# Optimization experiments

Hardware: AMD Instinct MI355X
Metric: run time of the kernel (lower is better)

Reference implementation:

```python
import jax, jax.numpy as jnp
import numpy as np

N_QUBITS = 14
N_LAYERS = 4
N_CLASSES = 10
BATCH = 1024


def apply_1q(state, gate, wire):
    """Apply a 2x2 gate ([2,2] shared or [B,2,2] batched) to `wire` of state [B,2,...,2]."""
    s = jnp.moveaxis(state, wire + 1, -1)
    shp = s.shape
    s = s.reshape(shp[0], -1, 2)
    if gate.ndim == 3:
        s = jnp.einsum('bij,bkj->bki', gate, s)
    else:
        s = jnp.einsum('ij,bkj->bki', gate, s)
    return jnp.moveaxis(s.reshape(shp), -1, wire + 1)


def apply_cnot(state, c, t):
    s = jnp.moveaxis(state, (c + 1, t + 1), (-2, -1))
    s = jnp.stack([s[..., 0, :], s[..., 1, ::-1]], axis=-2)
    return jnp.moveaxis(s, (-2, -1), (c + 1, t + 1))


def simulate(x, q_params):
    """Batched statevector sim of: RY(x_i) embed -> BasicEntanglerLayers(RX + CNOT ring) -> <Z_i>."""
    B, n = x.shape
    state = jnp.zeros((B,) + (2,) * n, jnp.complex64)
    state = state.at[(slice(None),) + (0,) * n].set(1.0)

    # RY(x_i) on each wire (angles batched per sample)
    c, s = jnp.cos(0.5 * x), jnp.sin(0.5 * x)
    for w in range(n):
        g = jnp.stack([jnp.stack([c[:, w], -s[:, w]], -1),
                       jnp.stack([s[:, w], c[:, w]], -1)], -2).astype(jnp.complex64)  # [B,2,2]
        state = apply_1q(state, g, w)

    # BasicEntanglerLayers: per layer RX(weights[l,i]) on every wire, then CNOT ring
    cw, sw = jnp.cos(0.5 * q_params), jnp.sin(0.5 * q_params)
    n_layers = q_params.shape[0]
    for l in range(n_layers):
        for w in range(n):
            cc = cw[l, w].astype(jnp.complex64)
            isw = (-1j) * sw[l, w].astype(jnp.complex64)
            g = jnp.stack([jnp.stack([cc, isw]), jnp.stack([isw, cc])])  # [2,2] RX
            state = apply_1q(state, g, w)
        if n == 2:
            state = apply_cnot(state, 0, 1)
        else:
            for w in range(n):
                state = apply_cnot(state, w, (w + 1) % n)

    # <Z_i> = P(bit_i=0) - P(bit_i=1)
    p = jnp.abs(state) ** 2  # [B,2,...,2] real
    axes_all = tuple(range(1, n + 1))
    z = []
    for w in range(n):
        pw = jnp.sum(p, axis=tuple(a for a in axes_all if a != w + 1))  # [B,2]
        z.append(pw[:, 0] - pw[:, 1])
    return jnp.stack(z, -1).astype(jnp.float32)  # [B, n]


def setup_inputs() -> dict:
    key = jax.random.key(0)
    k1, k2, k3, k4 = jax.random.split(key, 4)
    x = jax.random.normal(k1, (BATCH, N_QUBITS), dtype=jnp.float32)
    q_params = 0.01 * jax.random.normal(k2, (N_LAYERS, N_QUBITS), dtype=jnp.float32)
    fc_w = jax.random.normal(k3, (N_CLASSES, N_QUBITS), dtype=jnp.float32) / np.sqrt(N_QUBITS)
    fc_b = jax.random.normal(k4, (N_CLASSES,), dtype=jnp.float32) * 0.01
    return {"x": x, "q_params": q_params, "fc_w": fc_w, "fc_b": fc_b}


def reference(x, q_params, fc_w, fc_b):
    q_out = simulate(x, q_params)            # [B, n_qubits]
    logits = q_out @ fc_w.T + fc_b           # [B, n_classes]
    return logits
```

## Files before the change

### kernel.cpp

```cpp
#include <hip/hip_runtime.h>
#include <hip/hip_fp16.h>
#include <math.h>


#define NQ 14
#define NLAYERS 4
#define NCLASSES 10
#define BLOCK 512

typedef _Float16 f16;
typedef _Float16 f16x8 __attribute__((ext_vector_type(8)));
typedef _Float16 f16x4 __attribute__((ext_vector_type(4)));
typedef float f32x4 __attribute__((ext_vector_type(4)));
typedef unsigned int u32;
typedef u32 u32x4 __attribute__((ext_vector_type(4)));

__device__ __forceinline__ f32x4 mf(f16x8 a, f16x8 b, f32x4 c) {
  return __builtin_amdgcn_mfma_f32_16x16x32_f16(a, b, c, 0, 0, 0);
}

__device__ __forceinline__ int finv5(int n) {
  n ^= ((n >> 3) & 1) << 4;
  n ^= ((n >> 2) & 1) << 3;
  n ^= ((n >> 1) & 1) << 2;
  n ^= (n & 1) << 1;
  return n;
}
__device__ __forceinline__ int finv3(int n) {
  n ^= ((n >> 2) & 1) << 3;
  n ^= ((n >> 1) & 1) << 2;
  n ^= (n & 1) << 1;
  return n;
}

__device__ __forceinline__ void splitB(f16x8 b, int s, f16x8& br, f16x8& bi) {
  u32x4 u = __builtin_bit_cast(u32x4, b);
  const u32 m0 = s ? 0xFFFF0000u : 0x0000FFFFu;
  const u32 m1 = s ? 0x0000FFFFu : 0xFFFF0000u;
  u32x4 r;
  r[0] = u[0] & m0; r[1] = u[1] & m1; r[2] = u[2] & m1; r[3] = u[3] & m0;
  u32x4 ii;
  ii[0] = u[0] ^ r[0]; ii[1] = u[1] ^ r[1]; ii[2] = u[2] ^ r[2]; ii[3] = u[3] ^ r[3];
  br = __builtin_bit_cast(f16x8, r);
  bi = __builtin_bit_cast(f16x8, ii);
}

__device__ __forceinline__ void build32(f16* Bc, const float* qc, const float* qs,
                                        int base, int tid) {
  const float c0 = qc[base], c1 = qc[base+1], c2 = qc[base+2], c3 = qc[base+3], c4 = qc[base+4];
  const float s0 = qs[base], s1 = qs[base+1], s2 = qs[base+2], s3 = qs[base+3], s4 = qs[base+4];
#pragma unroll
  for (int e = tid; e < 1024; e += BLOCK) {
    const int n = e >> 5, k = e & 31;
    const int d = finv5(n) ^ k;
    float mag = ((d & 1) ? s0 : c0) * ((d & 2) ? s1 : c1);
    mag *= ((d & 4) ? s2 : c2) * ((d & 8) ? s3 : c3);
    mag *= ((d & 16) ? s4 : c4);
    const int t = __popc(d) & 3;
    Bc[n * 32 + k] = (f16)((t == 1 || t == 2) ? -mag : mag);
  }
}

__device__ __forceinline__ void buildC(f16* Bc, const float* qc, const float* qs,
                                       int base, int tid) {
  const float c0 = qc[base], c1 = qc[base+1], c2 = qc[base+2], c3 = qc[base+3];
  const float s0 = qs[base], s1 = qs[base+1], s2 = qs[base+2], s3 = qs[base+3];
  if (tid < 512) {
    const int n = tid >> 5, k = tid & 31;
    float v = 0.f;
    if (k < 16) {
      const int d = finv3(n) ^ k;
      float mag = ((d & 1) ? s0 : c0) * ((d & 2) ? s1 : c1);
      mag *= ((d & 4) ? s2 : c2) * ((d & 8) ? s3 : c3);
      const int t = __popc(d) & 3;
      v = (t == 1 || t == 2) ? -mag : mag;
    }
    Bc[n * 32 + k] = (f16)v;
  }
}

template<bool CTRL>
__device__ __forceinline__ void pass32(f16* __restrict__ reP, f16* __restrict__ imP,
                                       const f16* __restrict__ Bc, int tid) {
  const int lane = tid & 63, wave = tid >> 6;
  const int q = lane >> 4, cc = lane & 15;
  int n0 = cc, n1 = cc | 16;
  if (CTRL && wave >= 4) { n0 ^= 31; n1 ^= 31; }
  const int pq = (0x6 >> q) & 1;
  f16x8 br0, bi0, br1, bi1;
  {
    const f16x8 b0 = *(const f16x8*)(Bc + n0 * 32 + 8 * q);
    const f16x8 b1 = *(const f16x8*)(Bc + n1 * 32 + 8 * q);
    splitB(b0, ((n0 >> 4) ^ pq) & 1, br0, bi0);
    splitB(b1, ((n1 >> 4) ^ pq) & 1, br1, bi1);
  }
  f16x4 outR[8], outI[8];
#pragma unroll
  for (int i = 0; i < 4; ++i) {
    const int mt = wave * 4 + i;
    const int pA = ((mt * 16 + cc) * 32 + 8 * q) ^ ((mt & 7) << 3);
    const f16x8 Ar = *(const f16x8*)(reP + pA);
    const f16x8 Ai = *(const f16x8*)(imP + pA);
    const f16x8 nAi = -Ai;
#pragma unroll
    for (int nt = 0; nt < 2; ++nt) {
      const f16x8 br = nt ? br1 : br0;
      const f16x8 bi = nt ? bi1 : bi0;
      f32x4 aR = {0.f, 0.f, 0.f, 0.f}, aI = {0.f, 0.f, 0.f, 0.f};
      aR = mf(Ar, br, aR); aR = mf(nAi, bi, aR);
      aI = mf(Ar, bi, aI); aI = mf(Ai, br, aI);
      outR[i * 2 + nt] = __builtin_convertvector(aR, f16x4);
      outI[i * 2 + nt] = __builtin_convertvector(aI, f16x4);
    }
  }
  __syncthreads();
#pragma unroll
  for (int i = 0; i < 4; ++i) {
#pragma unroll
    for (int nt = 0; nt < 2; ++nt) {
      const int n5 = nt * 16 + cc;
      const int rr = (wave * 4 + i) * 16 + 4 * q;
      const int pS = (rr | (n5 << 9)) ^ ((n5 & 7) << 3);
      *(f16x4*)(reP + pS) = outR[i * 2 + nt];
      *(f16x4*)(imP + pS) = outI[i * 2 + nt];
    }
  }
}

template<bool FINAL>
__device__ __forceinline__ void passC(f16* __restrict__ reP, f16* __restrict__ imP,
                                      const f16* __restrict__ Bc, int tid,
                                      float* __restrict__ zloc) {
  const int lane = tid & 63, wave = tid >> 6;
  const int q = lane >> 4, cc = lane & 15;
  int n0 = cc;
  if (wave >= 4) n0 ^= 15;
  const int pq = (0x6 >> q) & 1;
  f16x8 br, bi;
  {
    const f16x8 b = *(const f16x8*)(Bc + n0 * 32 + 8 * q);
    splitB(b, ((n0 >> 3) ^ pq) & 1, br, bi);
  }
  f16x4 outR[8], outI[8];
#pragma unroll
  for (int i = 0; i < 8; ++i) {
    const int mt = wave * 8 + i;
    const int pA = ((mt * 16 + cc) * 16 + 8 * (q & 1)) ^ (((mt >> 1) & 7) << 3);
    const f16x8 Ar = *(const f16x8*)(reP + pA);
    const f16x8 Ai = *(const f16x8*)(imP + pA);
    const f16x8 nAi = -Ai;
    f32x4 aR = {0.f, 0.f, 0.f, 0.f}, aI = {0.f, 0.f, 0.f, 0.f};
    aR = mf(Ar, br, aR); aR = mf(nAi, bi, aR);
    aI = mf(Ar, bi, aI); aI = mf(Ai, br, aI);
    if constexpr (FINAL) {
      float p0 = aR[0]*aR[0] + aI[0]*aI[0];
      float p1 = aR[1]*aR[1] + aI[1]*aI[1];
      float p2 = aR[2]*aR[2] + aI[2]*aI[2];
      float p3 = aR[3]*aR[3] + aI[3]*aI[3];
      if (cc & 8) { float t = p0; p0 = p1; p1 = t; t = p2; p2 = p3; p3 = t; }
      const float ps = p0 + p1 + p2 + p3;
      zloc[0] += (p0 - p1) + (p2 - p3);
      zloc[1] += (p0 + p1) - (p2 + p3);
      zloc[2] += (q & 1) ? -ps : ps;
      zloc[3] += (q & 2) ? -ps : ps;
#pragma unroll
      for (int w = 0; w < 6; ++w) zloc[4 + w] += ((mt >> w) & 1) ? -ps : ps;
#pragma unroll
      for (int w = 0; w < 4; ++w) zloc[10 + w] += ((cc >> w) & 1) ? -ps : ps;
    } else {
      if (cc & 8) {
        f32x4 tR = aR, tI = aI;
        aR[0] = tR[1]; aR[1] = tR[0]; aR[2] = tR[3]; aR[3] = tR[2];
        aI[0] = tI[1]; aI[1] = tI[0]; aI[2] = tI[3]; aI[3] = tI[2];
      }
      outR[i] = __builtin_convertvector(aR, f16x4);
      outI[i] = __builtin_convertvector(aI, f16x4);
    }
  }
  if constexpr (!FINAL) {
    __syncthreads();
#pragma unroll
    for (int i = 0; i < 8; ++i) {
      const int rr = (wave * 8 + i) * 16 + 4 * q;
      const int nI = rr | (cc << 10);
      const int pS = nI ^ ((((rr >> 9) | ((cc & 3) << 1)) & 7) << 3);
      *(f16x4*)(reP + pS) = outR[i];
      *(f16x4*)(imP + pS) = outI[i];
    }
  }
}

__global__ __launch_bounds__(BLOCK, 4) void qsim_kernel(
    const float* __restrict__ x, const float* __restrict__ qp,
    const float* __restrict__ fcw, const float* __restrict__ fcb,
    float* __restrict__ out) {
  extern __shared__ unsigned char smem[];
  f16* reP = (f16*)smem;
  f16* imP = reP + 16384;
  unsigned char* scr = (unsigned char*)(imP + 16384);
  f16* Bc = (f16*)scr;
  float* qc = (float*)(scr + 2048);
  float* qs = qc + 56;
  float* xc = qs + 56;
  float* xs = xc + 14;

  const int b = blockIdx.x;
  const int tid = threadIdx.x;

  if (tid < NQ) {
    float sv, cv; sincosf(0.5f * x[b * NQ + tid], &sv, &cv);
    xc[tid] = cv; xs[tid] = sv;
  } else if (tid >= 64 && tid < 64 + NLAYERS * NQ) {
    const int k = tid - 64;
    float sv, cv; sincosf(0.5f * qp[k], &sv, &cv);
    qc[k] = cv; qs[k] = sv;
  }
  __syncthreads();

  float* Flo  = (float*)scr;
  float* psi  = Flo + 32;
  float* PsiR = psi + 32;
  float* PsiI = PsiR + 32;
  if (tid < 32) {
    float f = 1.f;
#pragma unroll
    for (int j = 0; j < 5; ++j) f *= ((tid >> j) & 1) ? xs[5 + j] : xc[5 + j];
    Flo[tid] = f;
  } else if (tid < 64) {
    const int k = tid - 32;
    float f = 1.f;
#pragma unroll
    for (int j = 0; j < 5; ++j) f *= ((k >> j) & 1) ? xs[j] : xc[j];
    psi[k] = f;
  }
  __syncthreads();
  if (tid < 32) {
    const float c0 = qc[0], c1 = qc[1], c2 = qc[2], c3 = qc[3], c4 = qc[4];
    const float s0 = qs[0], s1 = qs[1], s2 = qs[2], s3 = qs[3], s4 = qs[4];
    const int a = finv5(tid);
    float ar = 0.f, ai = 0.f;
    for (int k = 0; k < 32; ++k) {
      const int d = a ^ k;
      float mag = ((d & 1) ? s0 : c0) * ((d & 2) ? s1 : c1);
      mag *= ((d & 4) ? s2 : c2) * ((d & 8) ? s3 : c3);
      mag *= ((d & 16) ? s4 : c4);
      mag *= psi[k];
      const int t = __popc(d) & 3;
      if (t == 0) ar += mag; else if (t == 1) ai -= mag;
      else if (t == 2) ar -= mag; else ai += mag;
    }
    PsiR[tid] = ar; PsiI[tid] = ai;
  }
  __syncthreads();
  {
    float fhi = 1.f;
#pragma unroll
    for (int j = 0; j < 4; ++j) fhi *= ((tid >> j) & 1) ? xs[10 + j] : xc[10 + j];
    const float cr = fhi * PsiR[tid >> 4], ci = fhi * PsiI[tid >> 4];
    const int pconst = ((tid >> 4) & 7) << 3;
#pragma unroll
    for (int kb = 0; kb < 4; ++kb) {
      f16x8 hr, hi;
#pragma unroll
      for (int j = 0; j < 8; ++j) {
        const float F = Flo[8 * kb + j];
        hr[j] = (f16)(F * cr);
        hi[j] = (f16)(F * ci);
      }
      const int pb = (tid * 32 + 8 * kb) ^ pconst;
      *(f16x8*)(reP + pb) = hr;
      *(f16x8*)(imP + pb) = hi;
    }
  }
  __syncthreads();

  build32(Bc, qc, qs, 0 * NQ + 5, tid);  __syncthreads();
  pass32<true>(reP, imP, Bc, tid);       __syncthreads();
  buildC(Bc, qc, qs, 0 * NQ + 10, tid);  __syncthreads();
  passC<false>(reP, imP, Bc, tid, nullptr); __syncthreads();
#pragma unroll
  for (int l = 1; l < 3; ++l) {
    build32(Bc, qc, qs, l * NQ + 0, tid);  __syncthreads();
    pass32<false>(reP, imP, Bc, tid);      __syncthreads();
    build32(Bc, qc, qs, l * NQ + 5, tid);  __syncthreads();
    pass32<true>(reP, imP, Bc, tid);       __syncthreads();
    buildC(Bc, qc, qs, l * NQ + 10, tid);  __syncthreads();
    passC<false>(reP, imP, Bc, tid, nullptr); __syncthreads();
  }
  build32(Bc, qc, qs, 3 * NQ + 0, tid);  __syncthreads();
  pass32<false>(reP, imP, Bc, tid);      __syncthreads();
  build32(Bc, qc, qs, 3 * NQ + 5, tid);  __syncthreads();
  pass32<true>(reP, imP, Bc, tid);       __syncthreads();
  buildC(Bc, qc, qs, 3 * NQ + 10, tid);  __syncthreads();

  float zloc[NQ];
#pragma unroll
  for (int w = 0; w < NQ; ++w) zloc[w] = 0.f;
  passC<true>(reP, imP, Bc, tid, zloc);
  __syncthreads();

  float* zpart = (float*)scr;
  float* zbuf  = zpart + 112;
#pragma unroll
  for (int w = 0; w < NQ; ++w) {
#pragma unroll
    for (int off = 32; off > 0; off >>= 1)
      zloc[w] += __shfl_down(zloc[w], off, 64);
  }
  const int wave = tid >> 6, lane = tid & 63;
  if (lane == 0) {
#pragma unroll
    for (int w = 0; w < NQ; ++w) zpart[wave * NQ + w] = zloc[w];
  }
  __syncthreads();
  if (tid < NQ) {
    float a = 0.f;
#pragma unroll
    for (int v = 0; v < 8; ++v) a += zpart[v * NQ + tid];
    zbuf[tid] = a;
  }
  __syncthreads();
  if (tid < NCLASSES) {
    float acc = fcb[tid];
#pragma unroll
    for (int w = 0; w < NQ; ++w) acc = fmaf(zbuf[w], fcw[tid * NQ + w], acc);
    out[b * NCLASSES + tid] = acc;
  }
}

extern "C" void kernel_launch(void* const* d_in, const int* in_sizes, int n_in,
                              void* d_out, int out_size, void* d_ws, size_t ws_size,
                              hipStream_t stream) {
  const float* x   = (const float*)d_in[0];
  const float* qp  = (const float*)d_in[1];
  const float* fcw = (const float*)d_in[2];
  const float* fcb = (const float*)d_in[3];
  float* out = (float*)d_out;
  const int B = in_sizes[0] / NQ;

  const size_t shmem = 65536 + 2048 + 448 + 112;
  (void)hipFuncSetAttribute((const void*)qsim_kernel,
                            hipFuncAttributeMaxDynamicSharedMemorySize, (int)shmem);
  qsim_kernel<<<B, BLOCK, shmem, stream>>>(x, qp, fcw, fcb, out);
}
```

Baseline: 146.1 us.

## Double-buffer gate matrices and overlap gate build with MFMA passes; new LDS swizzle

Gate matrices are now built into a second LDS buffer inside each pass, between the MFMA compute and the barrier, instead of in separate build-then-sync phases. This removes roughly one barrier per pass and hides the build ALU work behind MFMA latency. The state and gate LDS layouts are reorganised with a new XOR swizzle to change bank-conflict behaviour on the A loads and scattered stores. The negation moves from the A operand to the B fragment so it is computed once per pass. The risks are higher register pressure and layout-index bugs.

```diff
diff --git a/kernel.cpp b/kernel.cpp
--- a/kernel.cpp
+++ b/kernel.cpp
@@ -18,6 +18,7 @@
 __device__ __forceinline__ f32x4 mf(f16x8 a, f16x8 b, f32x4 c) {
   return __builtin_amdgcn_mfma_f32_16x16x32_f16(a, b, c, 0, 0, 0);
 }
+__device__ __forceinline__ int swz(int t) { return ((t ^ (t >> 3)) & 7) << 3; }
 
 __device__ __forceinline__ int finv5(int n) {
   n ^= ((n >> 3) & 1) << 4;
@@ -57,10 +58,9 @@
     mag *= ((d & 4) ? s2 : c2) * ((d & 8) ? s3 : c3);
     mag *= ((d & 16) ? s4 : c4);
     const int t = __popc(d) & 3;
-    Bc[n * 32 + k] = (f16)((t == 1 || t == 2) ? -mag : mag);
-  }
-}
-
+    Bc[256 * (k >> 3) + 8 * n + (k & 7)] = (f16)((t == 1 || t == 2) ? -mag : mag);
+  }
+}
 __device__ __forceinline__ void buildC(f16* Bc, const float* qc, const float* qs,
                                        int base, int tid) {
   const float c0 = qc[base], c1 = qc[base+1], c2 = qc[base+2], c3 = qc[base+3];
@@ -75,13 +75,15 @@
       const int t = __popc(d) & 3;
       v = (t == 1 || t == 2) ? -mag : mag;
     }
-    Bc[n * 32 + k] = (f16)v;
-  }
-}
-
-template<bool CTRL>
+    Bc[256 * (k >> 3) + 8 * n + (k & 7)] = (f16)v;
+  }
+}
+
+template<bool CTRL, bool STORE_C, int BUILD>
 __device__ __forceinline__ void pass32(f16* __restrict__ reP, f16* __restrict__ imP,
-                                       const f16* __restrict__ Bc, int tid) {
+                                       const f16* __restrict__ BcR, f16* __restrict__ BcW,
+                                       const float* __restrict__ qc,
+                                       const float* __restrict__ qs, int bbase, int tid) {
   const int lane = tid & 63, wave = tid >> 6;
   const int q = lane >> 4, cc = lane & 15;
   int n0 = cc, n1 = cc | 16;
@@ -89,47 +91,61 @@
   const int pq = (0x6 >> q) & 1;
   f16x8 br0, bi0, br1, bi1;
   {
-    const f16x8 b0 = *(const f16x8*)(Bc + n0 * 32 + 8 * q);
-    const f16x8 b1 = *(const f16x8*)(Bc + n1 * 32 + 8 * q);
+    const f16x8 b0 = *(const f16x8*)(BcR + 256 * q + 8 * n0);
+    const f16x8 b1 = *(const f16x8*)(BcR + 256 * q + 8 * n1);
     splitB(b0, ((n0 >> 4) ^ pq) & 1, br0, bi0);
     splitB(b1, ((n1 >> 4) ^ pq) & 1, br1, bi1);
   }
+  const f16x8 nbi0 = -bi0, nbi1 = -bi1;
   f16x4 outR[8], outI[8];
 #pragma unroll
   for (int i = 0; i < 4; ++i) {
     const int mt = wave * 4 + i;
-    const int pA = ((mt * 16 + cc) * 32 + 8 * q) ^ ((mt & 7) << 3);
+    const int pA = mt * 512 + ((128 * q + 8 * cc) ^ swz(mt));
     const f16x8 Ar = *(const f16x8*)(reP + pA);
     const f16x8 Ai = *(const f16x8*)(imP + pA);
-    const f16x8 nAi = -Ai;
-#pragma unroll
-    for (int nt = 0; nt < 2; ++nt) {
-      const f16x8 br = nt ? br1 : br0;
-      const f16x8 bi = nt ? bi1 : bi0;
-      f32x4 aR = {0.f, 0.f, 0.f, 0.f}, aI = {0.f, 0.f, 0.f, 0.f};
-      aR = mf(Ar, br, aR); aR = mf(nAi, bi, aR);
-      aI = mf(Ar, bi, aI); aI = mf(Ai, br, aI);
-      outR[i * 2 + nt] = __builtin_convertvector(aR, f16x4);
-      outI[i * 2 + nt] = __builtin_convertvector(aI, f16x4);
-    }
-  }
+    {
+      f32x4 aR = {0.f,0.f,0.f,0.f}, aI = {0.f,0.f,0.f,0.f};
+      aR = mf(Ar, br0, aR); aR = mf(Ai, nbi0, aR);
+      aI = mf(Ar, bi0, aI); aI = mf(Ai, br0, aI);
+      outR[i * 2 + 0] = __builtin_convertvector(aR, f16x4);
+      outI[i * 2 + 0] = __builtin_convertvector(aI, f16x4);
+    }
+    {
+      f32x4 aR = {0.f,0.f,0.f,0.f}, aI = {0.f,0.f,0.f,0.f};
+      aR = mf(Ar, br1, aR); aR = mf(Ai, nbi1, aR);
+      aI = mf(Ar, bi1, aI); aI = mf(Ai, br1, aI);
+      outR[i * 2 + 1] = __builtin_convertvector(aR, f16x4);
+      outI[i * 2 + 1] = __builtin_convertvector(aI, f16x4);
+    }
+  }
+  if constexpr (BUILD == 1) build32(BcW, qc, qs, bbase, tid);
+  else if constexpr (BUILD == 2) buildC(BcW, qc, qs, bbase, tid);
   __syncthreads();
 #pragma unroll
   for (int i = 0; i < 4; ++i) {
+    const int mt = wave * 4 + i;
 #pragma unroll
     for (int nt = 0; nt < 2; ++nt) {
       const int n5 = nt * 16 + cc;
-      const int rr = (wave * 4 + i) * 16 + 4 * q;
-      const int pS = (rr | (n5 << 9)) ^ ((n5 & 7) << 3);
+      int pS;
+      if constexpr (STORE_C) {
+        const int tC = (mt >> 4) + 2 * n5;
+        pS = tC * 256 + ((128 * (q >> 1) + 8 * (mt & 15) + 4 * (q & 1)) ^ swz(tC));
+      } else {
+        pS = n5 * 512 + ((128 * (2 * (mt & 1) + (q >> 1)) + 8 * (mt >> 1) + 4 * (q & 1)) ^ swz(n5));
+      }
       *(f16x4*)(reP + pS) = outR[i * 2 + nt];
       *(f16x4*)(imP + pS) = outI[i * 2 + nt];
     }
   }
 }
 
-template<bool FINAL>
+template<bool FINAL, int BUILD>
 __device__ __forceinline__ void passC(f16* __restrict__ reP, f16* __restrict__ imP,
-                                      const f16* __restrict__ Bc, int tid,
+                                      const f16* __restrict__ BcR, f16* __restrict__ BcW,
+                                      const float* __restrict__ qc,
+                                      const float* __restrict__ qs, int bbase, int tid,
                                       float* __restrict__ zloc) {
   const int lane = tid & 63, wave = tid >> 6;
   const int q = lane >> 4, cc = lane & 15;
@@ -138,19 +154,19 @@
   const int pq = (0x6 >> q) & 1;
   f16x8 br, bi;
   {
-    const f16x8 b = *(const f16x8*)(Bc + n0 * 32 + 8 * q);
+    const f16x8 b = *(const f16x8*)(BcR + 256 * q + 8 * n0);
     splitB(b, ((n0 >> 3) ^ pq) & 1, br, bi);
   }
+  const f16x8 nbi = -bi;
   f16x4 outR[8], outI[8];
 #pragma unroll
   for (int i = 0; i < 8; ++i) {
-    const int mt = wave * 8 + i;
-    const int pA = ((mt * 16 + cc) * 16 + 8 * (q & 1)) ^ (((mt >> 1) & 7) << 3);
+    const int mtC = wave * 8 + i;
+    const int pA = mtC * 256 + ((128 * (q & 1) + 8 * cc) ^ swz(mtC));
     const f16x8 Ar = *(const f16x8*)(reP + pA);
     const f16x8 Ai = *(const f16x8*)(imP + pA);
-    const f16x8 nAi = -Ai;
-    f32x4 aR = {0.f, 0.f, 0.f, 0.f}, aI = {0.f, 0.f, 0.f, 0.f};
-    aR = mf(Ar, br, aR); aR = mf(nAi, bi, aR);
+    f32x4 aR = {0.f,0.f,0.f,0.f}, aI = {0.f,0.f,0.f,0.f};
+    aR = mf(Ar, br, aR); aR = mf(Ai, nbi, aR);
     aI = mf(Ar, bi, aI); aI = mf(Ai, br, aI);
     if constexpr (FINAL) {
       float p0 = aR[0]*aR[0] + aI[0]*aI[0];
@@ -164,7 +180,7 @@
       zloc[2] += (q & 1) ? -ps : ps;
       zloc[3] += (q & 2) ? -ps : ps;
 #pragma unroll
-      for (int w = 0; w < 6; ++w) zloc[4 + w] += ((mt >> w) & 1) ? -ps : ps;
+      for (int w = 0; w < 6; ++w) zloc[4 + w] += ((mtC >> w) & 1) ? -ps : ps;
 #pragma unroll
       for (int w = 0; w < 4; ++w) zloc[10 + w] += ((cc >> w) & 1) ? -ps : ps;
     } else {
@@ -177,13 +193,15 @@
       outI[i] = __builtin_convertvector(aI, f16x4);
     }
   }
+  if constexpr (BUILD == 1) build32(BcW, qc, qs, bbase, tid);
   if constexpr (!FINAL) {
     __syncthreads();
 #pragma unroll
     for (int i = 0; i < 8; ++i) {
-      const int rr = (wave * 8 + i) * 16 + 4 * q;
-      const int nI = rr | (cc << 10);
-      const int pS = nI ^ ((((rr >> 9) | ((cc & 3) << 1)) & 7) << 3);
+      const int mtC = wave * 8 + i;
+      const int tP = 2 * cc + (mtC >> 5);
+      const int pS = tP * 512 +
+          ((128 * (2 * (mtC & 1) + (q >> 1)) + 8 * ((mtC >> 1) & 15) + 4 * (q & 1)) ^ swz(tP));
       *(f16x4*)(reP + pS) = outR[i];
       *(f16x4*)(imP + pS) = outI[i];
     }
@@ -197,9 +215,9 @@
   extern __shared__ unsigned char smem[];
   f16* reP = (f16*)smem;
   f16* imP = reP + 16384;
-  unsigned char* scr = (unsigned char*)(imP + 16384);
-  f16* Bc = (f16*)scr;
-  float* qc = (float*)(scr + 2048);
+  f16* Bc0 = imP + 16384;
+  f16* Bc1 = Bc0 + 1024;
+  float* qc = (float*)(Bc1 + 1024);
   float* qs = qc + 56;
   float* xc = qs + 56;
   float* xs = xc + 14;
@@ -217,10 +235,11 @@
   }
   __syncthreads();
 
-  float* Flo  = (float*)scr;
+  float* Flo  = (float*)Bc1;
   float* psi  = Flo + 32;
   float* PsiR = psi + 32;
   float* PsiI = PsiR + 32;
+  build32(Bc0, qc, qs, 0 * NQ + 5, tid);
   if (tid < 32) {
     float f = 1.f;
 #pragma unroll
@@ -257,7 +276,8 @@
 #pragma unroll
     for (int j = 0; j < 4; ++j) fhi *= ((tid >> j) & 1) ? xs[10 + j] : xc[10 + j];
     const float cr = fhi * PsiR[tid >> 4], ci = fhi * PsiI[tid >> 4];
-    const int pconst = ((tid >> 4) & 7) << 3;
+    const int t = tid >> 4;
+    const int sz = swz(t);
 #pragma unroll
     for (int kb = 0; kb < 4; ++kb) {
       f16x8 hr, hi;
@@ -267,39 +287,31 @@
         hr[j] = (f16)(F * cr);
         hi[j] = (f16)(F * ci);
       }
-      const int pb = (tid * 32 + 8 * kb) ^ pconst;
+      const int pb = t * 512 + ((128 * kb + 8 * (tid & 15)) ^ sz);
       *(f16x8*)(reP + pb) = hr;
       *(f16x8*)(imP + pb) = hi;
     }
   }
   __syncthreads();
 
-  build32(Bc, qc, qs, 0 * NQ + 5, tid);  __syncthreads();
-  pass32<true>(reP, imP, Bc, tid);       __syncthreads();
-  buildC(Bc, qc, qs, 0 * NQ + 10, tid);  __syncthreads();
-  passC<false>(reP, imP, Bc, tid, nullptr); __syncthreads();
-#pragma unroll
-  for (int l = 1; l < 3; ++l) {
-    build32(Bc, qc, qs, l * NQ + 0, tid);  __syncthreads();
-    pass32<false>(reP, imP, Bc, tid);      __syncthreads();
-    build32(Bc, qc, qs, l * NQ + 5, tid);  __syncthreads();
-    pass32<true>(reP, imP, Bc, tid);       __syncthreads();
-    buildC(Bc, qc, qs, l * NQ + 10, tid);  __syncthreads();
-    passC<false>(reP, imP, Bc, tid, nullptr); __syncthreads();
-  }
-  build32(Bc, qc, qs, 3 * NQ + 0, tid);  __syncthreads();
-  pass32<false>(reP, imP, Bc, tid);      __syncthreads();
-  build32(Bc, qc, qs, 3 * NQ + 5, tid);  __syncthreads();
-  pass32<true>(reP, imP, Bc, tid);       __syncthreads();
-  buildC(Bc, qc, qs, 3 * NQ + 10, tid);  __syncthreads();
+  pass32<true,  true,  2>(reP, imP, Bc0, Bc1, qc, qs, 0*NQ+10, tid); __syncthreads();
+  passC <false, 1>(reP, imP, Bc1, Bc0, qc, qs, 1*NQ+0,  tid, nullptr); __syncthreads();
+  pass32<false, false, 1>(reP, imP, Bc0, Bc1, qc, qs, 1*NQ+5,  tid); __syncthreads();
+  pass32<true,  true,  2>(reP, imP, Bc1, Bc0, qc, qs, 1*NQ+10, tid); __syncthreads();
+  passC <false, 1>(reP, imP, Bc0, Bc1, qc, qs, 2*NQ+0,  tid, nullptr); __syncthreads();
+  pass32<false, false, 1>(reP, imP, Bc1, Bc0, qc, qs, 2*NQ+5,  tid); __syncthreads();
+  pass32<true,  true,  2>(reP, imP, Bc0, Bc1, qc, qs, 2*NQ+10, tid); __syncthreads();
+  passC <false, 1>(reP, imP, Bc1, Bc0, qc, qs, 3*NQ+0,  tid, nullptr); __syncthreads();
+  pass32<false, false, 1>(reP, imP, Bc0, Bc1, qc, qs, 3*NQ+5,  tid); __syncthreads();
+  pass32<true,  true,  2>(reP, imP, Bc1, Bc0, qc, qs, 3*NQ+10, tid); __syncthreads();
 
   float zloc[NQ];
 #pragma unroll
   for (int w = 0; w < NQ; ++w) zloc[w] = 0.f;
-  passC<true>(reP, imP, Bc, tid, zloc);
-  __syncthreads();
-
-  float* zpart = (float*)scr;
+  passC<true, 0>(reP, imP, Bc0, Bc1, qc, qs, 0, tid, zloc);
+  __syncthreads();
+
+  float* zpart = (float*)Bc0;
   float* zbuf  = zpart + 112;
 #pragma unroll
   for (int w = 0; w < NQ; ++w) {
@@ -338,7 +350,8 @@
   float* out = (float*)d_out;
   const int B = in_sizes[0] / NQ;
 
-  const size_t shmem = 65536 + 2048 + 448 + 112;
+  const size_t shmem = (size_t)(2 * 16384 + 2 * 1024) * sizeof(f16)
+                     + (size_t)(56 + 56 + 14 + 14) * sizeof(float);
   (void)hipFuncSetAttribute((const void*)qsim_kernel,
                             hipFuncAttributeMaxDynamicSharedMemorySize, (int)shmem);
   qsim_kernel<<<B, BLOCK, shmem, stream>>>(x, qp, fcw, fcb, out);
```

New measurement: 141.5 us. 1.03x faster.
